# Kernel tuning notes

Measured on AMD Instinct MI355X. Metric: run time of the kernel, lower is better.

## Reference

```python
import jax, jax.numpy as jnp
import numpy as np

N = 6144          # number_of_nodes
E = 196608        # random edges (self-loops appended in reference, as add_self_loops does)
L_GAT = 10        # GAT num_layers
NEG_SLOPE = 0.2   # GATConv leaky_relu slope


def setup_inputs() -> dict:
    key = jax.random.key(0)
    ks = jax.random.split(key, 27)
    g = lambda i, shape, s=0.3: jax.random.normal(ks[i], shape, jnp.float32) * s
    return {
        "x": jax.random.normal(ks[0], (N, 3), jnp.float32),
        "mask": jax.random.uniform(ks[1], (N,), dtype=jnp.float32),
        "edge_index": jax.random.randint(ks[2], (2, E), 0, N),
        # 10-layer GAT (heads=1): per-layer lin weight, att_src, att_dst, bias
        "gat_W": g(3, (L_GAT, 3, 3)), "gat_asrc": g(4, (L_GAT, 3)),
        "gat_adst": g(5, (L_GAT, 3)), "gat_b": g(6, (L_GAT, 3), 0.1),
        # nn.MultiheadAttention(embed_dim=3, num_heads=3)
        "mha_in_w": g(7, (9, 3)), "mha_in_b": g(8, (9,), 0.1),
        "mha_out_w": g(9, (3, 3)), "mha_out_b": g(10, (3,), 0.1),
        # TransformerConv(3, 3, heads=1)
        "tc_Wq": g(11, (3, 3)), "tc_bq": g(12, (3,), 0.1),
        "tc_Wk": g(13, (3, 3)), "tc_bk": g(14, (3,), 0.1),
        "tc_Wv": g(15, (3, 3)), "tc_bv": g(16, (3,), 0.1),
        "tc_Wskip": g(17, (3, 3)), "tc_bskip": g(18, (3,), 0.1),
        # actor MLP: Linear(3N,16) -> ReLU -> Linear(16,32) -> ReLU -> Linear(32,N)
        "mlp_W1": g(19, (3 * N, 16), 0.02), "mlp_b1": g(20, (16,), 0.1),
        "mlp_W2": g(21, (16, 32), 0.2), "mlp_b2": g(22, (32,), 0.1),
        "mlp_W3": g(23, (32, N), 0.2), "mlp_b3": jnp.zeros((N,), jnp.float32),
        # critic Linear(1,1)
        "critic_W": g(24, (1, 1)), "critic_b": g(25, (1,), 0.1),
    }


def _seg_softmax(e, seg, n):
    # numerically-stable softmax grouped by destination node
    m = jax.lax.stop_gradient(jax.ops.segment_max(e, seg, num_segments=n))
    w = jnp.exp(e - m[seg])
    z = jax.ops.segment_sum(w, seg, num_segments=n)
    return w / (z[seg] + 1e-16)


def reference(x, mask, edge_index, gat_W, gat_asrc, gat_adst, gat_b,
              mha_in_w, mha_in_b, mha_out_w, mha_out_b,
              tc_Wq, tc_bq, tc_Wk, tc_bk, tc_Wv, tc_bv, tc_Wskip, tc_bskip,
              mlp_W1, mlp_b1, mlp_W2, mlp_b2, mlp_W3, mlp_b3,
              critic_W, critic_b):
    n = x.shape[0]
    loops = jnp.arange(n)
    src = jnp.concatenate([edge_index[0], loops])  # add_self_loops
    dst = jnp.concatenate([edge_index[1], loops])

    # ---- 10-layer GAT (heads=1, ReLU between layers) ----
    h = x
    for l in range(L_GAT):
        xp = h @ gat_W[l]                                   # [N,3]
        e = jax.nn.leaky_relu(xp[src] @ gat_asrc[l] + xp[dst] @ gat_adst[l], NEG_SLOPE)
        alpha = _seg_softmax(e, dst, n)
        h_new = jax.ops.segment_sum(alpha[:, None] * xp[src], dst, num_segments=n) + gat_b[l]
        h = jax.nn.relu(h_new) if l < L_GAT - 1 else h_new

    # ---- MultiheadAttention(embed_dim=3, num_heads=3 => head_dim=1), history = [h] ----
    qkv = h @ mha_in_w.T + mha_in_b                         # [N,9]
    q, k, v = qkv[:, 0:3], qkv[:, 3:6], qkv[:, 6:9]
    scores = jnp.einsum('nh,mh->hnm', q, k)                 # head_dim=1 -> scale = 1
    attn = jax.nn.softmax(scores, axis=-1)                  # [3,N,N] -- dominant memory
    o = jnp.einsum('hnm,mh->nh', attn, v)                   # [N,3]
    h2 = o @ mha_out_w.T + mha_out_b

    # ---- TransformerConv(3, 3, heads=1) ----
    q2 = h2 @ tc_Wq + tc_bq
    k2 = h2 @ tc_Wk + tc_bk
    v2 = h2 @ tc_Wv + tc_bv
    logit = (q2[dst] * k2[src]).sum(-1) * (1.0 / np.sqrt(3.0))
    alpha2 = _seg_softmax(logit, dst, n)
    agg = jax.ops.segment_sum(alpha2[:, None] * v2[src], dst, num_segments=n)
    h3 = agg + h2 @ tc_Wskip + tc_bskip                     # root_weight skip

    # ---- actor MLP over flattened node features ----
    flat = h3.reshape(-1)                                   # [3N]
    a1 = jax.nn.relu(flat @ mlp_W1 + mlp_b1)
    a2 = jax.nn.relu(a1 @ mlp_W2 + mlp_b2)
    results = (a2 @ mlp_W3 + mlp_b3)[:, None]               # [N,1]

    new_results = results[:, 0] * mask
    value = jnp.mean(results @ critic_W + critic_b)
    return new_results, value
```

## Files before the change

### kernel.cpp

```cpp
#include <hip/hip_runtime.h>

#define N 6144
#define E 196608
#define EN (E + N)
#define LGAT 10

typedef unsigned int u32;

__device__ __forceinline__ u32 f2key(float f) {
    u32 u = __float_as_uint(f);
    return (u & 0x80000000u) ? ~u : (u | 0x80000000u);
}
__device__ __forceinline__ float key2f(u32 k) {
    u32 u = (k & 0x80000000u) ? (k & 0x7FFFFFFFu) : ~k;
    return __uint_as_float(u);
}

struct P {
    const float *x, *mask, *gat_W, *gat_asrc, *gat_adst, *gat_b;
    const float *in_w, *in_b, *out_w, *out_b;
    const float *Wq, *bq, *Wk, *bk, *Wv, *bv, *Wsk, *bsk;
    const float *W1, *b1, *W2, *b2, *W3, *b3, *cW, *cb;
    const int *src, *dst;
    float *xp, *ssrc, *sdst, *h, *qkv, *qkv2, *h2, *h3, *numden;
    float *a1pre, *a2buf, *sumres;
    u32 *deg, *offs, *cursor, *kmaxk, *kmink;
    int *ssorted;
    float *out;
};

__global__ void k_init(P p) {
    int t = blockIdx.x * 256 + threadIdx.x;
    if (t < N) p.deg[t] = 0u;
    if (t < 3) p.kmaxk[t] = 0u;
    else if (t < 6) p.kmink[t - 3] = 0xFFFFFFFFu;
    else if (t < 22) p.a1pre[t - 6] = 0.f;
    else if (t == 22) p.sumres[0] = 0.f;
}

__global__ void k_hist(P p) {
    int e = blockIdx.x * 256 + threadIdx.x;
    if (e >= EN) return;
    int d = (e < E) ? p.dst[e] : (e - E);
    atomicAdd(&p.deg[d], 1u);
}

__global__ void k_scan(P p) {
    __shared__ u32 part[256];
    int t = threadIdx.x;
    u32 loc[24];
    u32 sum = 0;
    #pragma unroll
    for (int i = 0; i < 24; ++i) { loc[i] = sum; sum += p.deg[t * 24 + i]; }
    part[t] = sum;
    __syncthreads();
    for (int o = 1; o < 256; o <<= 1) {
        u32 v = (t >= o) ? part[t - o] : 0u;
        __syncthreads();
        part[t] += v;
        __syncthreads();
    }
    u32 base = (t == 0) ? 0u : part[t - 1];
    #pragma unroll
    for (int i = 0; i < 24; ++i) {
        u32 off = base + loc[i];
        p.offs[t * 24 + i] = off;
        p.cursor[t * 24 + i] = off;
    }
    if (t == 255) p.offs[N] = part[255];
}

__global__ void k_scatter(P p) {
    int e = blockIdx.x * 256 + threadIdx.x;
    if (e >= EN) return;
    int s = (e < E) ? p.src[e] : (e - E);
    int d = (e < E) ? p.dst[e] : (e - E);
    u32 pos = atomicAdd(&p.cursor[d], 1u);
    p.ssorted[pos] = s;
}

__global__ void k_gat_node(P p, int l) {
    int n = blockIdx.x * 256 + threadIdx.x;
    const float* hp = (l == 0) ? p.x : p.h;
    float h0 = hp[n * 3 + 0], h1 = hp[n * 3 + 1], h2 = hp[n * 3 + 2];
    const float* W = p.gat_W + l * 9;
    float xp0 = h0 * W[0] + h1 * W[3] + h2 * W[6];
    float xp1 = h0 * W[1] + h1 * W[4] + h2 * W[7];
    float xp2 = h0 * W[2] + h1 * W[5] + h2 * W[8];
    p.xp[n * 3 + 0] = xp0; p.xp[n * 3 + 1] = xp1; p.xp[n * 3 + 2] = xp2;
    const float* as = p.gat_asrc + l * 3;
    const float* ad = p.gat_adst + l * 3;
    p.ssrc[n] = xp0 * as[0] + xp1 * as[1] + xp2 * as[2];
    p.sdst[n] = xp0 * ad[0] + xp1 * ad[1] + xp2 * ad[2];
}

__global__ void k_gat_edge(P p, int l) {
    int gid = blockIdx.x * 256 + threadIdx.x;
    int d = gid >> 4;
    int lane = gid & 15;
    u32 beg = p.offs[d], end = p.offs[d + 1];
    float sd = p.sdst[d];
    float mx = -1e30f;
    for (u32 i = beg + lane; i < end; i += 16) {
        float v = p.ssrc[p.ssorted[i]] + sd;
        v = (v >= 0.f) ? v : 0.2f * v;
        mx = fmaxf(mx, v);
    }
    #pragma unroll
    for (int o = 1; o < 16; o <<= 1) mx = fmaxf(mx, __shfl_xor(mx, o));
    float sz = 0.f, s0 = 0.f, s1 = 0.f, s2 = 0.f;
    for (u32 i = beg + lane; i < end; i += 16) {
        int s = p.ssorted[i];
        float v = p.ssrc[s] + sd;
        v = (v >= 0.f) ? v : 0.2f * v;
        float w = __expf(v - mx);
        sz += w;
        s0 += w * p.xp[s * 3 + 0];
        s1 += w * p.xp[s * 3 + 1];
        s2 += w * p.xp[s * 3 + 2];
    }
    #pragma unroll
    for (int o = 1; o < 16; o <<= 1) {
        sz += __shfl_xor(sz, o);
        s0 += __shfl_xor(s0, o);
        s1 += __shfl_xor(s1, o);
        s2 += __shfl_xor(s2, o);
    }
    if (lane == 0) {
        float z = sz + 1e-16f;
        float b0 = p.gat_b[l * 3 + 0], b1 = p.gat_b[l * 3 + 1], b2 = p.gat_b[l * 3 + 2];
        float o0 = s0 / z + b0, o1 = s1 / z + b1, o2 = s2 / z + b2;
        if (l < LGAT - 1) { o0 = fmaxf(o0, 0.f); o1 = fmaxf(o1, 0.f); o2 = fmaxf(o2, 0.f); }
        p.h[d * 3 + 0] = o0; p.h[d * 3 + 1] = o1; p.h[d * 3 + 2] = o2;
    }
}

__global__ void k_qkv(P p) {
    int n = blockIdx.x * 256 + threadIdx.x;
    float h0 = p.h[n * 3 + 0], h1 = p.h[n * 3 + 1], h2 = p.h[n * 3 + 2];
    float kk[3];
    #pragma unroll
    for (int j = 0; j < 9; ++j) {
        float v = h0 * p.in_w[j * 3 + 0] + h1 * p.in_w[j * 3 + 1] +
                  h2 * p.in_w[j * 3 + 2] + p.in_b[j];
        p.qkv[n * 9 + j] = v;
        if (j >= 3 && j < 6) kk[j - 3] = v;
    }
    #pragma unroll
    for (int j = 0; j < 6; ++j) p.numden[n * 6 + j] = 0.f;
    #pragma unroll
    for (int hh = 0; hh < 3; ++hh) {
        float mx = kk[hh], mn = kk[hh];
        #pragma unroll
        for (int o = 32; o; o >>= 1) {
            mx = fmaxf(mx, __shfl_xor(mx, o));
            mn = fminf(mn, __shfl_xor(mn, o));
        }
        if ((threadIdx.x & 63) == 0) {
            atomicMax(&p.kmaxk[hh], f2key(mx));
            atomicMin(&p.kmink[hh], f2key(mn));
        }
    }
}

#define MCH 384
__global__ void k_att_partial(P p) {
    __shared__ float kv[MCH * 6];
    int tid = threadIdx.x;
    int chunk = blockIdx.y;
    int mbase = chunk * MCH;
    for (int i = tid; i < MCH * 6; i += 256) {
        int mm = i / 6, r = i - mm * 6;
        kv[i] = p.qkv[(mbase + mm) * 9 + 3 + r];
    }
    __syncthreads();
    int n = blockIdx.x * 256 + tid;
    float q0 = p.qkv[n * 9 + 0], q1 = p.qkv[n * 9 + 1], q2 = p.qkv[n * 9 + 2];
    float kmx0 = key2f(p.kmaxk[0]), kmx1 = key2f(p.kmaxk[1]), kmx2 = key2f(p.kmaxk[2]);
    float kmn0 = key2f(p.kmink[0]), kmn1 = key2f(p.kmink[1]), kmn2 = key2f(p.kmink[2]);
    float M0 = (q0 >= 0.f) ? q0 * kmx0 : q0 * kmn0;
    float M1 = (q1 >= 0.f) ? q1 * kmx1 : q1 * kmn1;
    float M2 = (q2 >= 0.f) ? q2 * kmx2 : q2 * kmn2;
    float num0 = 0, den0 = 0, num1 = 0, den1 = 0, num2 = 0, den2 = 0;
    for (int mm = 0; mm < MCH; ++mm) {
        float k0 = kv[mm * 6 + 0], k1 = kv[mm * 6 + 1], k2 = kv[mm * 6 + 2];
        float v0 = kv[mm * 6 + 3], v1 = kv[mm * 6 + 4], v2 = kv[mm * 6 + 5];
        float t0 = __expf(q0 * k0 - M0); den0 += t0; num0 += t0 * v0;
        float t1 = __expf(q1 * k1 - M1); den1 += t1; num1 += t1 * v1;
        float t2 = __expf(q2 * k2 - M2); den2 += t2; num2 += t2 * v2;
    }
    float* nd = p.numden + n * 6;
    atomicAdd(&nd[0], num0); atomicAdd(&nd[1], den0);
    atomicAdd(&nd[2], num1); atomicAdd(&nd[3], den1);
    atomicAdd(&nd[4], num2); atomicAdd(&nd[5], den2);
}

__global__ void k_att_reduce(P p) {
    int n = blockIdx.x * 256 + threadIdx.x;
    float o[3];
    #pragma unroll
    for (int hh = 0; hh < 3; ++hh)
        o[hh] = p.numden[n * 6 + hh * 2] / p.numden[n * 6 + hh * 2 + 1];
    float h2v[3];
    #pragma unroll
    for (int c = 0; c < 3; ++c) {
        h2v[c] = p.out_b[c] + o[0] * p.out_w[c * 3 + 0] +
                 o[1] * p.out_w[c * 3 + 1] + o[2] * p.out_w[c * 3 + 2];
        p.h2[n * 3 + c] = h2v[c];
    }
    #pragma unroll
    for (int c = 0; c < 3; ++c) {
        float q2 = p.bq[c] + h2v[0] * p.Wq[c] + h2v[1] * p.Wq[3 + c] + h2v[2] * p.Wq[6 + c];
        float k2 = p.bk[c] + h2v[0] * p.Wk[c] + h2v[1] * p.Wk[3 + c] + h2v[2] * p.Wk[6 + c];
        float v2 = p.bv[c] + h2v[0] * p.Wv[c] + h2v[1] * p.Wv[3 + c] + h2v[2] * p.Wv[6 + c];
        p.qkv2[n * 9 + c] = q2;
        p.qkv2[n * 9 + 3 + c] = k2;
        p.qkv2[n * 9 + 6 + c] = v2;
    }
}

__global__ void k_tc_edge(P p) {
    int gid = blockIdx.x * 256 + threadIdx.x;
    int d = gid >> 4;
    int lane = gid & 15;
    u32 beg = p.offs[d], end = p.offs[d + 1];
    float q0 = p.qkv2[d * 9 + 0], q1 = p.qkv2[d * 9 + 1], q2 = p.qkv2[d * 9 + 2];
    const float RS3 = 0.57735026919f;
    float mx = -1e30f;
    for (u32 i = beg + lane; i < end; i += 16) {
        int s = p.ssorted[i];
        float lg = (q0 * p.qkv2[s * 9 + 3] + q1 * p.qkv2[s * 9 + 4] +
                    q2 * p.qkv2[s * 9 + 5]) * RS3;
        mx = fmaxf(mx, lg);
    }
    #pragma unroll
    for (int o = 1; o < 16; o <<= 1) mx = fmaxf(mx, __shfl_xor(mx, o));
    float sz = 0.f, s0 = 0.f, s1 = 0.f, s2 = 0.f;
    for (u32 i = beg + lane; i < end; i += 16) {
        int s = p.ssorted[i];
        float lg = (q0 * p.qkv2[s * 9 + 3] + q1 * p.qkv2[s * 9 + 4] +
                    q2 * p.qkv2[s * 9 + 5]) * RS3;
        float w = __expf(lg - mx);
        sz += w;
        s0 += w * p.qkv2[s * 9 + 6];
        s1 += w * p.qkv2[s * 9 + 7];
        s2 += w * p.qkv2[s * 9 + 8];
    }
    #pragma unroll
    for (int o = 1; o < 16; o <<= 1) {
        sz += __shfl_xor(sz, o);
        s0 += __shfl_xor(s0, o);
        s1 += __shfl_xor(s1, o);
        s2 += __shfl_xor(s2, o);
    }
    if (lane == 0) {
        float z = sz + 1e-16f;
        float h0 = p.h2[d * 3 + 0], h1 = p.h2[d * 3 + 1], h2 = p.h2[d * 3 + 2];
        #pragma unroll
        for (int c = 0; c < 3; ++c) {
            float agg = (c == 0 ? s0 : (c == 1 ? s1 : s2)) / z;
            p.h3[d * 3 + c] = agg + p.bsk[c] +
                h0 * p.Wsk[c] + h1 * p.Wsk[3 + c] + h2 * p.Wsk[6 + c];
        }
    }
}

__global__ void k_mlp1(P p) {
    int g = blockIdx.x * 256 + threadIdx.x;
    float acc[16];
    #pragma unroll
    for (int j = 0; j < 16; ++j) acc[j] = 0.f;
    for (int i = g; i < 3 * N; i += 6144) {
        float f = p.h3[i];
        const float* w = p.W1 + (size_t)i * 16;
        #pragma unroll
        for (int j = 0; j < 16; ++j) acc[j] += f * w[j];
    }
    #pragma unroll
    for (int o = 32; o; o >>= 1)
        #pragma unroll
        for (int j = 0; j < 16; ++j) acc[j] += __shfl_xor(acc[j], o);
    if ((threadIdx.x & 63) == 0)
        #pragma unroll
        for (int j = 0; j < 16; ++j) atomicAdd(&p.a1pre[j], acc[j]);
}

__global__ void k_mlp2(P p) {
    __shared__ float a1[16];
    int t = threadIdx.x;
    if (t < 16) a1[t] = fmaxf(p.a1pre[t] + p.b1[t], 0.f);
    __syncthreads();
    if (t < 32) {
        float acc = p.b2[t];
        #pragma unroll
        for (int i = 0; i < 16; ++i) acc += a1[i] * p.W2[i * 32 + t];
        p.a2buf[t] = fmaxf(acc, 0.f);
    }
}

__global__ void k_mlp3(P p) {
    __shared__ float a2[32];
    if (threadIdx.x < 32) a2[threadIdx.x] = p.a2buf[threadIdx.x];
    __syncthreads();
    int n = blockIdx.x * 256 + threadIdx.x;
    float acc = p.b3[n];
    #pragma unroll
    for (int j = 0; j < 32; ++j) acc += a2[j] * p.W3[(size_t)j * N + n];
    p.out[n] = acc * p.mask[n];
    float s = acc;
    #pragma unroll
    for (int o = 32; o; o >>= 1) s += __shfl_xor(s, o);
    if ((threadIdx.x & 63) == 0) atomicAdd(p.sumres, s);
}

__global__ void k_value(P p) {
    p.out[N] = p.cW[0] * (p.sumres[0] / (float)N) + p.cb[0];
}

extern "C" void kernel_launch(void* const* d_in, const int* in_sizes, int n_in,
                              void* d_out, int out_size, void* d_ws, size_t ws_size,
                              hipStream_t stream) {
    P p;
    p.x      = (const float*)d_in[0];
    p.mask   = (const float*)d_in[1];
    const int* ei = (const int*)d_in[2];
    p.src = ei; p.dst = ei + E;
    p.gat_W  = (const float*)d_in[3];
    p.gat_asrc = (const float*)d_in[4];
    p.gat_adst = (const float*)d_in[5];
    p.gat_b  = (const float*)d_in[6];
    p.in_w   = (const float*)d_in[7];
    p.in_b   = (const float*)d_in[8];
    p.out_w  = (const float*)d_in[9];
    p.out_b  = (const float*)d_in[10];
    p.Wq = (const float*)d_in[11]; p.bq = (const float*)d_in[12];
    p.Wk = (const float*)d_in[13]; p.bk = (const float*)d_in[14];
    p.Wv = (const float*)d_in[15]; p.bv = (const float*)d_in[16];
    p.Wsk = (const float*)d_in[17]; p.bsk = (const float*)d_in[18];
    p.W1 = (const float*)d_in[19]; p.b1 = (const float*)d_in[20];
    p.W2 = (const float*)d_in[21]; p.b2 = (const float*)d_in[22];
    p.W3 = (const float*)d_in[23]; p.b3 = (const float*)d_in[24];
    p.cW = (const float*)d_in[25]; p.cb = (const float*)d_in[26];

    float* ws = (float*)d_ws;
    p.xp      = ws + 0;
    p.ssrc    = ws + 18432;
    p.sdst    = ws + 24576;
    p.h       = ws + 30720;
    p.qkv     = ws + 49152;
    p.qkv2    = ws + 104448;
    p.h2      = ws + 159744;
    p.h3      = ws + 178176;
    p.numden  = ws + 196608;
    p.deg     = (u32*)(ws + 233472);
    p.offs    = (u32*)(ws + 239616);
    p.cursor  = (u32*)(ws + 245761);
    p.ssorted = (int*)(ws + 251905);
    p.a1pre   = ws + 454657;
    p.a2buf   = ws + 454673;
    p.sumres  = ws + 454705;
    p.kmaxk   = (u32*)(ws + 454706);
    p.kmink   = (u32*)(ws + 454709);
    p.out     = (float*)d_out;

    k_init<<<24, 256, 0, stream>>>(p);
    k_hist<<<792, 256, 0, stream>>>(p);
    k_scan<<<1, 256, 0, stream>>>(p);
    k_scatter<<<792, 256, 0, stream>>>(p);
    for (int l = 0; l < LGAT; ++l) {
        k_gat_node<<<24, 256, 0, stream>>>(p, l);
        k_gat_edge<<<384, 256, 0, stream>>>(p, l);
    }
    k_qkv<<<24, 256, 0, stream>>>(p);
    k_att_partial<<<dim3(24, 16), 256, 0, stream>>>(p);
    k_att_reduce<<<24, 256, 0, stream>>>(p);
    k_tc_edge<<<384, 256, 0, stream>>>(p);
    k_mlp1<<<24, 256, 0, stream>>>(p);
    k_mlp2<<<1, 64, 0, stream>>>(p);
    k_mlp3<<<24, 256, 0, stream>>>(p);
    k_value<<<1, 1, 0, stream>>>(p);
}
```

Measured before the change: 301.9 us.

## Fuse GAT node transforms into edge kernel, pack node features, drop atomics

Each GAT layer's next-layer linear transform and attention scores are computed in the edge kernel's epilogue, with ping-pong float4 node buffers packing features and the source score. This removes the per-layer node kernel launch and cuts scattered gather loads. Edge kernels now use 32 lanes per destination, attention partials are written to a chunked buffer and reduced without atomics (chunk size halved, more blocks), TC key/value are packed into float4s, and mlp1 is restructured with more blocks and shared-memory reduction. Init work also moves into the scan kernel to save work in k_init. The partial buffer adds workspace and extra reduction reads.

```diff
diff --git a/kernel.cpp b/kernel.cpp
--- a/kernel.cpp
+++ b/kernel.cpp
@@ -22,7 +22,10 @@
     const float *Wq, *bq, *Wk, *bk, *Wv, *bv, *Wsk, *bsk;
     const float *W1, *b1, *W2, *b2, *W3, *b3, *cW, *cb;
     const int *src, *dst;
-    float *xp, *ssrc, *sdst, *h, *qkv, *qkv2, *h2, *h3, *numden;
+    float4 *nodeA, *nodeB;
+    float *sdstA, *sdstB;
+    float *qkv, *q2, *h2, *h3, *part;
+    float4 *kv2;
     float *a1pre, *a2buf, *sumres;
     u32 *deg, *offs, *cursor, *kmaxk, *kmink;
     int *ssorted;
@@ -32,10 +35,6 @@
 __global__ void k_init(P p) {
     int t = blockIdx.x * 256 + threadIdx.x;
     if (t < N) p.deg[t] = 0u;
-    if (t < 3) p.kmaxk[t] = 0u;
-    else if (t < 6) p.kmink[t - 3] = 0xFFFFFFFFu;
-    else if (t < 22) p.a1pre[t - 6] = 0.f;
-    else if (t == 22) p.sumres[0] = 0.f;
 }
 
 __global__ void k_hist(P p) {
@@ -48,6 +47,10 @@
 __global__ void k_scan(P p) {
     __shared__ u32 part[256];
     int t = threadIdx.x;
+    if (t < 3) p.kmaxk[t] = 0u;
+    else if (t < 6) p.kmink[t - 3] = 0xFFFFFFFFu;
+    else if (t < 22) p.a1pre[t - 6] = 0.f;
+    else if (t == 22) p.sumres[0] = 0.f;
     u32 loc[24];
     u32 sum = 0;
     #pragma unroll
@@ -79,48 +82,47 @@
     p.ssorted[pos] = s;
 }
 
-__global__ void k_gat_node(P p, int l) {
+__global__ void k_node0(P p) {
     int n = blockIdx.x * 256 + threadIdx.x;
-    const float* hp = (l == 0) ? p.x : p.h;
-    float h0 = hp[n * 3 + 0], h1 = hp[n * 3 + 1], h2 = hp[n * 3 + 2];
-    const float* W = p.gat_W + l * 9;
+    float h0 = p.x[n * 3 + 0], h1 = p.x[n * 3 + 1], h2 = p.x[n * 3 + 2];
+    const float* W = p.gat_W;
     float xp0 = h0 * W[0] + h1 * W[3] + h2 * W[6];
     float xp1 = h0 * W[1] + h1 * W[4] + h2 * W[7];
     float xp2 = h0 * W[2] + h1 * W[5] + h2 * W[8];
-    p.xp[n * 3 + 0] = xp0; p.xp[n * 3 + 1] = xp1; p.xp[n * 3 + 2] = xp2;
-    const float* as = p.gat_asrc + l * 3;
-    const float* ad = p.gat_adst + l * 3;
-    p.ssrc[n] = xp0 * as[0] + xp1 * as[1] + xp2 * as[2];
-    p.sdst[n] = xp0 * ad[0] + xp1 * ad[1] + xp2 * ad[2];
-}
-
-__global__ void k_gat_edge(P p, int l) {
+    float ss = xp0 * p.gat_asrc[0] + xp1 * p.gat_asrc[1] + xp2 * p.gat_asrc[2];
+    p.nodeA[n] = make_float4(xp0, xp1, xp2, ss);
+    p.sdstA[n] = xp0 * p.gat_adst[0] + xp1 * p.gat_adst[1] + xp2 * p.gat_adst[2];
+}
+
+__global__ void k_gat_edge(P p, const float4* __restrict__ nin,
+                           const float* __restrict__ sdin,
+                           float4* __restrict__ nout, float* __restrict__ sdout,
+                           int l) {
     int gid = blockIdx.x * 256 + threadIdx.x;
-    int d = gid >> 4;
-    int lane = gid & 15;
+    int d = gid >> 5;
+    int lane = gid & 31;
     u32 beg = p.offs[d], end = p.offs[d + 1];
-    float sd = p.sdst[d];
+    float sd = sdin[d];
     float mx = -1e30f;
-    for (u32 i = beg + lane; i < end; i += 16) {
-        float v = p.ssrc[p.ssorted[i]] + sd;
+    for (u32 i = beg + lane; i < end; i += 32) {
+        float4 r = nin[p.ssorted[i]];
+        float v = r.w + sd;
         v = (v >= 0.f) ? v : 0.2f * v;
         mx = fmaxf(mx, v);
     }
     #pragma unroll
-    for (int o = 1; o < 16; o <<= 1) mx = fmaxf(mx, __shfl_xor(mx, o));
+    for (int o = 1; o < 32; o <<= 1) mx = fmaxf(mx, __shfl_xor(mx, o));
     float sz = 0.f, s0 = 0.f, s1 = 0.f, s2 = 0.f;
-    for (u32 i = beg + lane; i < end; i += 16) {
-        int s = p.ssorted[i];
-        float v = p.ssrc[s] + sd;
+    for (u32 i = beg + lane; i < end; i += 32) {
+        float4 r = nin[p.ssorted[i]];
+        float v = r.w + sd;
         v = (v >= 0.f) ? v : 0.2f * v;
         float w = __expf(v - mx);
         sz += w;
-        s0 += w * p.xp[s * 3 + 0];
-        s1 += w * p.xp[s * 3 + 1];
-        s2 += w * p.xp[s * 3 + 2];
-    }
-    #pragma unroll
-    for (int o = 1; o < 16; o <<= 1) {
+        s0 += w * r.x; s1 += w * r.y; s2 += w * r.z;
+    }
+    #pragma unroll
+    for (int o = 1; o < 32; o <<= 1) {
         sz += __shfl_xor(sz, o);
         s0 += __shfl_xor(s0, o);
         s1 += __shfl_xor(s1, o);
@@ -128,26 +130,36 @@
     }
     if (lane == 0) {
         float z = sz + 1e-16f;
-        float b0 = p.gat_b[l * 3 + 0], b1 = p.gat_b[l * 3 + 1], b2 = p.gat_b[l * 3 + 2];
-        float o0 = s0 / z + b0, o1 = s1 / z + b1, o2 = s2 / z + b2;
-        if (l < LGAT - 1) { o0 = fmaxf(o0, 0.f); o1 = fmaxf(o1, 0.f); o2 = fmaxf(o2, 0.f); }
-        p.h[d * 3 + 0] = o0; p.h[d * 3 + 1] = o1; p.h[d * 3 + 2] = o2;
-    }
-}
-
-__global__ void k_qkv(P p) {
+        float o0 = s0 / z + p.gat_b[l * 3 + 0];
+        float o1 = s1 / z + p.gat_b[l * 3 + 1];
+        float o2 = s2 / z + p.gat_b[l * 3 + 2];
+        if (l < LGAT - 1) {
+            o0 = fmaxf(o0, 0.f); o1 = fmaxf(o1, 0.f); o2 = fmaxf(o2, 0.f);
+            const float* W = p.gat_W + (l + 1) * 9;
+            float xp0 = o0 * W[0] + o1 * W[3] + o2 * W[6];
+            float xp1 = o0 * W[1] + o1 * W[4] + o2 * W[7];
+            float xp2 = o0 * W[2] + o1 * W[5] + o2 * W[8];
+            const float* as = p.gat_asrc + (l + 1) * 3;
+            const float* ad = p.gat_adst + (l + 1) * 3;
+            float ss = xp0 * as[0] + xp1 * as[1] + xp2 * as[2];
+            nout[d] = make_float4(xp0, xp1, xp2, ss);
+            sdout[d] = xp0 * ad[0] + xp1 * ad[1] + xp2 * ad[2];
+        } else {
+            #pragma unroll
+            for (int j = 0; j < 9; ++j) {
+                float v = o0 * p.in_w[j * 3 + 0] + o1 * p.in_w[j * 3 + 1] +
+                          o2 * p.in_w[j * 3 + 2] + p.in_b[j];
+                p.qkv[d * 9 + j] = v;
+            }
+        }
+    }
+}
+
+__global__ void k_kminmax(P p) {
     int n = blockIdx.x * 256 + threadIdx.x;
-    float h0 = p.h[n * 3 + 0], h1 = p.h[n * 3 + 1], h2 = p.h[n * 3 + 2];
     float kk[3];
     #pragma unroll
-    for (int j = 0; j < 9; ++j) {
-        float v = h0 * p.in_w[j * 3 + 0] + h1 * p.in_w[j * 3 + 1] +
-                  h2 * p.in_w[j * 3 + 2] + p.in_b[j];
-        p.qkv[n * 9 + j] = v;
-        if (j >= 3 && j < 6) kk[j - 3] = v;
-    }
-    #pragma unroll
-    for (int j = 0; j < 6; ++j) p.numden[n * 6 + j] = 0.f;
+    for (int hh = 0; hh < 3; ++hh) kk[hh] = p.qkv[n * 9 + 3 + hh];
     #pragma unroll
     for (int hh = 0; hh < 3; ++hh) {
         float mx = kk[hh], mn = kk[hh];
@@ -163,7 +175,7 @@
     }
 }
 
-#define MCH 384
+#define MCH 192
 __global__ void k_att_partial(P p) {
     __shared__ float kv[MCH * 6];
     int tid = threadIdx.x;
@@ -189,18 +201,25 @@
         float t1 = __expf(q1 * k1 - M1); den1 += t1; num1 += t1 * v1;
         float t2 = __expf(q2 * k2 - M2); den2 += t2; num2 += t2 * v2;
     }
-    float* nd = p.numden + n * 6;
-    atomicAdd(&nd[0], num0); atomicAdd(&nd[1], den0);
-    atomicAdd(&nd[2], num1); atomicAdd(&nd[3], den1);
-    atomicAdd(&nd[4], num2); atomicAdd(&nd[5], den2);
+    float* pp = p.part + (size_t)chunk * 6 * N + n;
+    pp[0] = num0; pp[N] = den0; pp[2 * N] = num1;
+    pp[3 * N] = den1; pp[4 * N] = num2; pp[5 * N] = den2;
 }
 
 __global__ void k_att_reduce(P p) {
     int n = blockIdx.x * 256 + threadIdx.x;
+    float num[3] = {0.f, 0.f, 0.f}, den[3] = {0.f, 0.f, 0.f};
+    for (int c = 0; c < 32; ++c) {
+        const float* pp = p.part + (size_t)c * 6 * N + n;
+        #pragma unroll
+        for (int hh = 0; hh < 3; ++hh) {
+            num[hh] += pp[hh * 2 * N];
+            den[hh] += pp[(hh * 2 + 1) * N];
+        }
+    }
     float o[3];
     #pragma unroll
-    for (int hh = 0; hh < 3; ++hh)
-        o[hh] = p.numden[n * 6 + hh * 2] / p.numden[n * 6 + hh * 2 + 1];
+    for (int hh = 0; hh < 3; ++hh) o[hh] = num[hh] / den[hh];
     float h2v[3];
     #pragma unroll
     for (int c = 0; c < 3; ++c) {
@@ -208,46 +227,45 @@
                  o[1] * p.out_w[c * 3 + 1] + o[2] * p.out_w[c * 3 + 2];
         p.h2[n * 3 + c] = h2v[c];
     }
+    float q2v[3], k2v[3], v2v[3];
     #pragma unroll
     for (int c = 0; c < 3; ++c) {
-        float q2 = p.bq[c] + h2v[0] * p.Wq[c] + h2v[1] * p.Wq[3 + c] + h2v[2] * p.Wq[6 + c];
-        float k2 = p.bk[c] + h2v[0] * p.Wk[c] + h2v[1] * p.Wk[3 + c] + h2v[2] * p.Wk[6 + c];
-        float v2 = p.bv[c] + h2v[0] * p.Wv[c] + h2v[1] * p.Wv[3 + c] + h2v[2] * p.Wv[6 + c];
-        p.qkv2[n * 9 + c] = q2;
-        p.qkv2[n * 9 + 3 + c] = k2;
-        p.qkv2[n * 9 + 6 + c] = v2;
-    }
+        q2v[c] = p.bq[c] + h2v[0] * p.Wq[c] + h2v[1] * p.Wq[3 + c] + h2v[2] * p.Wq[6 + c];
+        k2v[c] = p.bk[c] + h2v[0] * p.Wk[c] + h2v[1] * p.Wk[3 + c] + h2v[2] * p.Wk[6 + c];
+        v2v[c] = p.bv[c] + h2v[0] * p.Wv[c] + h2v[1] * p.Wv[3 + c] + h2v[2] * p.Wv[6 + c];
+        p.q2[n * 3 + c] = q2v[c];
+    }
+    p.kv2[n * 2 + 0] = make_float4(k2v[0], k2v[1], k2v[2], v2v[0]);
+    p.kv2[n * 2 + 1] = make_float4(v2v[1], v2v[2], 0.f, 0.f);
 }
 
 __global__ void k_tc_edge(P p) {
     int gid = blockIdx.x * 256 + threadIdx.x;
-    int d = gid >> 4;
-    int lane = gid & 15;
+    int d = gid >> 5;
+    int lane = gid & 31;
     u32 beg = p.offs[d], end = p.offs[d + 1];
-    float q0 = p.qkv2[d * 9 + 0], q1 = p.qkv2[d * 9 + 1], q2 = p.qkv2[d * 9 + 2];
+    float q0 = p.q2[d * 3 + 0], q1 = p.q2[d * 3 + 1], q2 = p.q2[d * 3 + 2];
     const float RS3 = 0.57735026919f;
     float mx = -1e30f;
-    for (u32 i = beg + lane; i < end; i += 16) {
+    for (u32 i = beg + lane; i < end; i += 32) {
+        float4 ka = p.kv2[p.ssorted[i] * 2];
+        float lg = (q0 * ka.x + q1 * ka.y + q2 * ka.z) * RS3;
+        mx = fmaxf(mx, lg);
+    }
+    #pragma unroll
+    for (int o = 1; o < 32; o <<= 1) mx = fmaxf(mx, __shfl_xor(mx, o));
+    float sz = 0.f, s0 = 0.f, s1 = 0.f, s2 = 0.f;
+    for (u32 i = beg + lane; i < end; i += 32) {
         int s = p.ssorted[i];
-        float lg = (q0 * p.qkv2[s * 9 + 3] + q1 * p.qkv2[s * 9 + 4] +
-                    q2 * p.qkv2[s * 9 + 5]) * RS3;
-        mx = fmaxf(mx, lg);
-    }
-    #pragma unroll
-    for (int o = 1; o < 16; o <<= 1) mx = fmaxf(mx, __shfl_xor(mx, o));
-    float sz = 0.f, s0 = 0.f, s1 = 0.f, s2 = 0.f;
-    for (u32 i = beg + lane; i < end; i += 16) {
-        int s = p.ssorted[i];
-        float lg = (q0 * p.qkv2[s * 9 + 3] + q1 * p.qkv2[s * 9 + 4] +
-                    q2 * p.qkv2[s * 9 + 5]) * RS3;
+        float4 ka = p.kv2[s * 2];
+        float4 kb = p.kv2[s * 2 + 1];
+        float lg = (q0 * ka.x + q1 * ka.y + q2 * ka.z) * RS3;
         float w = __expf(lg - mx);
         sz += w;
-        s0 += w * p.qkv2[s * 9 + 6];
-        s1 += w * p.qkv2[s * 9 + 7];
-        s2 += w * p.qkv2[s * 9 + 8];
-    }
-    #pragma unroll
-    for (int o = 1; o < 16; o <<= 1) {
+        s0 += w * ka.w; s1 += w * kb.x; s2 += w * kb.y;
+    }
+    #pragma unroll
+    for (int o = 1; o < 32; o <<= 1) {
         sz += __shfl_xor(sz, o);
         s0 += __shfl_xor(s0, o);
         s1 += __shfl_xor(s1, o);
@@ -256,33 +274,35 @@
     if (lane == 0) {
         float z = sz + 1e-16f;
         float h0 = p.h2[d * 3 + 0], h1 = p.h2[d * 3 + 1], h2 = p.h2[d * 3 + 2];
+        float agg[3] = {s0 / z, s1 / z, s2 / z};
         #pragma unroll
         for (int c = 0; c < 3; ++c) {
-            float agg = (c == 0 ? s0 : (c == 1 ? s1 : s2)) / z;
-            p.h3[d * 3 + c] = agg + p.bsk[c] +
+            p.h3[d * 3 + c] = agg[c] + p.bsk[c] +
                 h0 * p.Wsk[c] + h1 * p.Wsk[3 + c] + h2 * p.Wsk[6 + c];
         }
     }
 }
 
 __global__ void k_mlp1(P p) {
-    int g = blockIdx.x * 256 + threadIdx.x;
-    float acc[16];
-    #pragma unroll
-    for (int j = 0; j < 16; ++j) acc[j] = 0.f;
-    for (int i = g; i < 3 * N; i += 6144) {
-        float f = p.h3[i];
-        const float* w = p.W1 + (size_t)i * 16;
-        #pragma unroll
-        for (int j = 0; j < 16; ++j) acc[j] += f * w[j];
-    }
-    #pragma unroll
-    for (int o = 32; o; o >>= 1)
-        #pragma unroll
-        for (int j = 0; j < 16; ++j) acc[j] += __shfl_xor(acc[j], o);
-    if ((threadIdx.x & 63) == 0)
-        #pragma unroll
-        for (int j = 0; j < 16; ++j) atomicAdd(&p.a1pre[j], acc[j]);
+    __shared__ float red[64];
+    int t = blockIdx.x * 256 + threadIdx.x;
+    int j = t & 15;
+    int g = t >> 4;
+    float acc = 0.f;
+    #pragma unroll
+    for (int k = 0; k < 16; ++k) {
+        int r = g + k * 1152;
+        acc += p.h3[r] * p.W1[r * 16 + j];
+    }
+    acc += __shfl_xor(acc, 16);
+    acc += __shfl_xor(acc, 32);
+    int tid = threadIdx.x;
+    if ((tid & 63) < 16) red[(tid >> 6) * 16 + j] = acc;
+    __syncthreads();
+    if (tid < 16) {
+        float s = red[tid] + red[16 + tid] + red[32 + tid] + red[48 + tid];
+        atomicAdd(&p.a1pre[tid], s);
+    }
 }
 
 __global__ void k_mlp2(P p) {
@@ -343,39 +363,44 @@
     p.cW = (const float*)d_in[25]; p.cb = (const float*)d_in[26];
 
     float* ws = (float*)d_ws;
-    p.xp      = ws + 0;
-    p.ssrc    = ws + 18432;
-    p.sdst    = ws + 24576;
-    p.h       = ws + 30720;
-    p.qkv     = ws + 49152;
-    p.qkv2    = ws + 104448;
-    p.h2      = ws + 159744;
-    p.h3      = ws + 178176;
-    p.numden  = ws + 196608;
-    p.deg     = (u32*)(ws + 233472);
-    p.offs    = (u32*)(ws + 239616);
-    p.cursor  = (u32*)(ws + 245761);
-    p.ssorted = (int*)(ws + 251905);
-    p.a1pre   = ws + 454657;
-    p.a2buf   = ws + 454673;
-    p.sumres  = ws + 454705;
-    p.kmaxk   = (u32*)(ws + 454706);
-    p.kmink   = (u32*)(ws + 454709);
+    p.nodeA   = (float4*)(ws + 0);
+    p.nodeB   = (float4*)(ws + 24576);
+    p.sdstA   = ws + 49152;
+    p.sdstB   = ws + 55296;
+    p.qkv     = ws + 61440;
+    p.q2      = ws + 116736;
+    p.kv2     = (float4*)(ws + 135168);
+    p.h2      = ws + 184320;
+    p.h3      = ws + 202752;
+    p.part    = ws + 221184;
+    p.a1pre   = ws + 1400832;
+    p.a2buf   = ws + 1400848;
+    p.sumres  = ws + 1400880;
+    p.kmaxk   = (u32*)(ws + 1400884);
+    p.kmink   = (u32*)(ws + 1400887);
+    p.deg     = (u32*)(ws + 1400890);
+    p.offs    = (u32*)(ws + 1407034);
+    p.cursor  = (u32*)(ws + 1413179);
+    p.ssorted = (int*)(ws + 1419323);
     p.out     = (float*)d_out;
 
     k_init<<<24, 256, 0, stream>>>(p);
     k_hist<<<792, 256, 0, stream>>>(p);
     k_scan<<<1, 256, 0, stream>>>(p);
     k_scatter<<<792, 256, 0, stream>>>(p);
+    k_node0<<<24, 256, 0, stream>>>(p);
     for (int l = 0; l < LGAT; ++l) {
-        k_gat_node<<<24, 256, 0, stream>>>(p, l);
-        k_gat_edge<<<384, 256, 0, stream>>>(p, l);
-    }
-    k_qkv<<<24, 256, 0, stream>>>(p);
-    k_att_partial<<<dim3(24, 16), 256, 0, stream>>>(p);
+        const float4* nin = (l & 1) ? p.nodeB : p.nodeA;
+        const float*  sdin = (l & 1) ? p.sdstB : p.sdstA;
+        float4* nout = (l & 1) ? p.nodeA : p.nodeB;
+        float*  sdout = (l & 1) ? p.sdstA : p.sdstB;
+        k_gat_edge<<<768, 256, 0, stream>>>(p, nin, sdin, nout, sdout, l);
+    }
+    k_kminmax<<<24, 256, 0, stream>>>(p);
+    k_att_partial<<<dim3(24, 32), 256, 0, stream>>>(p);
     k_att_reduce<<<24, 256, 0, stream>>>(p);
-    k_tc_edge<<<384, 256, 0, stream>>>(p);
-    k_mlp1<<<24, 256, 0, stream>>>(p);
+    k_tc_edge<<<768, 256, 0, stream>>>(p);
+    k_mlp1<<<72, 256, 0, stream>>>(p);
     k_mlp2<<<1, 64, 0, stream>>>(p);
     k_mlp3<<<24, 256, 0, stream>>>(p);
     k_value<<<1, 1, 0, stream>>>(p);
```

New measurement: 250.7 us. -17.0%, faster.
